# Performance work log

Hardware: AMD Instinct MI355X
Metric: run time of the kernel (lower is better)

## Reference

```python
import jax, jax.numpy as jnp
import numpy as np

DEPTH, HEADS, DH, BUCKET, NHASH = 4, 8, 64, 64, 4
DIM, VOCAB, BATCH, SEQ = 512, 50000, 2, 2048
LN_EPS = 1e-5
SELF_ATTN_VAL = -5e4  # TOKEN_SELF_ATTN_VALUE in reformer_pytorch


def layer_norm(x, s, b):
    mu = x.mean(-1, keepdims=True)
    var = ((x - mu) ** 2).mean(-1, keepdims=True)
    return (x - mu) / jnp.sqrt(var + LN_EPS) * s + b


def sincos(t, dh):
    # FixedPositionalEmbedding: emb = cat(sin, cos) of t x dh/2 angles
    inv = 1.0 / (10000.0 ** (jnp.arange(0, dh, 2, dtype=jnp.float32) / dh))
    ang = jnp.arange(t, dtype=jnp.float32)[:, None] * inv[None, :]
    return jnp.sin(ang), jnp.cos(ang)


def apply_rotary(qk, sin, cos):
    # qk: [B*H, T, DH]; sin/cos: [T, DH/2]; interleaved-pair rotary as in reformer_pytorch
    sin2 = jnp.repeat(sin, 2, axis=-1)[None]
    cos2 = jnp.repeat(cos, 2, axis=-1)[None]
    xr = qk.reshape(qk.shape[0], qk.shape[1], -1, 2)
    rot = jnp.stack((-xr[..., 1], xr[..., 0]), axis=-1).reshape(qk.shape)
    return qk * cos2 + rot * sin2


def lsh_attention(qk, v, rot):
    # qk, v: [B, T, dh] (B = batch*heads, shared-QK); rot: [dh, NHASH, n_buckets//2]
    B, T, dh = qk.shape
    nb = T // BUCKET
    rv = jnp.einsum('btf,fhi->bhti', qk, rot)           # [B, NHASH, T, nb/2]
    rv = jnp.concatenate([rv, -rv], axis=-1)
    buckets = jnp.argmax(rv, axis=-1)                    # [B, NHASH, T]
    buckets = (buckets + (jnp.arange(NHASH) * nb)[None, :, None]).reshape(B, NHASH * T)
    ticker = jnp.arange(NHASH * T) % T
    key = T * buckets + ticker[None, :]                  # unique sort keys
    sticker = jnp.argsort(key, axis=-1)                  # [B, NHASH*T]
    undo = jnp.argsort(sticker, axis=-1)
    st = sticker % T
    sqk = jnp.take_along_axis(qk, st[:, :, None], axis=1)
    sv = jnp.take_along_axis(v, st[:, :, None], axis=1)
    C = NHASH * nb                                       # num chunks, each BUCKET long
    bq_t = st.reshape(B, C, BUCKET)
    bq = sqk.reshape(B, C, BUCKET, dh)
    bv = sv.reshape(B, C, BUCKET, dh)
    bk = bq / jnp.maximum(jnp.linalg.norm(bq, axis=-1, keepdims=True), 1e-12)

    def look_one_back(a):
        return jnp.concatenate([a, jnp.roll(a, 1, axis=1)], axis=2)

    bk, bv, bkv_t = look_one_back(bk), look_one_back(bv), look_one_back(bq_t)
    dots = jnp.einsum('bcie,bcje->bcij', bq, bk) * (dh ** -0.5)
    dots = jnp.where(bq_t[:, :, :, None] == bkv_t[:, :, None, :], SELF_ATTN_VAL, dots)
    lse = jax.nn.logsumexp(dots, axis=-1, keepdims=True)
    p = jnp.exp(dots - lse)
    bo = jnp.einsum('bcij,bcje->bcie', p, bv)
    so = bo.reshape(B, NHASH * T, dh)
    slog = lse.reshape(B, NHASH * T)
    o = jnp.take_along_axis(so, undo[:, :, None], axis=1).reshape(B, NHASH, T, dh)
    lg = jnp.take_along_axis(slog, undo, axis=1).reshape(B, NHASH, T, 1)
    w = jnp.exp(lg - jax.nn.logsumexp(lg, axis=1, keepdims=True))
    return jnp.sum(o * w, axis=1)                        # [B, T, dh]


def attn_block(x, s, bln, Wqk, Wv, Wo, bo, rot, sin, cos):
    b, t, _ = x.shape
    xn = layer_norm(x, s, bln)
    qk = (xn @ Wqk).reshape(b, t, HEADS, DH).transpose(0, 2, 1, 3).reshape(b * HEADS, t, DH)
    v = (xn @ Wv).reshape(b, t, HEADS, DH).transpose(0, 2, 1, 3).reshape(b * HEADS, t, DH)
    qk = apply_rotary(qk, sin, cos)
    o = lsh_attention(qk, v, rot)
    o = o.reshape(b, HEADS, t, DH).transpose(0, 2, 1, 3).reshape(b, t, HEADS * DH)
    return o @ Wo + bo


def ff_block(x, s, b, W1, b1, W2, b2):
    xn = layer_norm(x, s, b)
    return jax.nn.gelu(xn @ W1 + b1, approximate=False) @ W2 + b2


def reference(x, token_emb, ln1_s, ln1_b, Wqk, Wv, Wo, bo, ln2_s, ln2_b, W1, b1, W2, b2, rotations, lnf_s, lnf_b, Wf1, bf1, Wout, bout):
    e = token_emb[x]                                     # [B, T, DIM]
    sin, cos = sincos(x.shape[1], DH)
    x1 = x2 = e                                          # reversible twin streams
    for i in range(DEPTH):
        x1 = x1 + attn_block(x2, ln1_s[i], ln1_b[i], Wqk[i], Wv[i], Wo[i], bo[i], rotations[i], sin, cos)
        x2 = x2 + ff_block(x1, ln2_s[i], ln2_b[i], W1[i], b1[i], W2[i], b2[i])
    h = layer_norm((x1 + x2) * 0.5, lnf_s, lnf_b)
    h = h.mean(axis=1)
    h = jax.nn.relu(h @ Wf1 + bf1)
    return h @ Wout + bout


def setup_inputs():
    key = jax.random.key(0)
    ks = jax.random.split(key, 10)
    nb = SEQ // BUCKET
    s = 0.02
    return {
        'x': jax.random.randint(ks[0], (BATCH, SEQ), 0, VOCAB),
        'token_emb': jax.random.normal(ks[1], (VOCAB, DIM), jnp.float32) * s,
        'ln1_s': jnp.ones((DEPTH, DIM), jnp.float32),
        'ln1_b': jnp.zeros((DEPTH, DIM), jnp.float32),
        'Wqk': jax.random.normal(ks[2], (DEPTH, DIM, HEADS * DH), jnp.float32) * s,
        'Wv': jax.random.normal(ks[3], (DEPTH, DIM, HEADS * DH), jnp.float32) * s,
        'Wo': jax.random.normal(ks[4], (DEPTH, HEADS * DH, DIM), jnp.float32) * s,
        'bo': jnp.zeros((DEPTH, DIM), jnp.float32),
        'ln2_s': jnp.ones((DEPTH, DIM), jnp.float32),
        'ln2_b': jnp.zeros((DEPTH, DIM), jnp.float32),
        'W1': jax.random.normal(ks[5], (DEPTH, DIM, 4 * DIM), jnp.float32) * s,
        'b1': jnp.zeros((DEPTH, 4 * DIM), jnp.float32),
        'W2': jax.random.normal(ks[6], (DEPTH, 4 * DIM, DIM), jnp.float32) * s,
        'b2': jnp.zeros((DEPTH, DIM), jnp.float32),
        'rotations': jax.random.normal(ks[7], (DEPTH, DH, NHASH, nb // 2), jnp.float32),
        'lnf_s': jnp.ones((DIM,), jnp.float32),
        'lnf_b': jnp.zeros((DIM,), jnp.float32),
        'Wf1': jax.random.normal(ks[8], (DIM, 256), jnp.float32) * s,
        'bf1': jnp.zeros((256,), jnp.float32),
        'Wout': jax.random.normal(ks[9], (256, 1), jnp.float32) * s,
        'bout': jnp.zeros((1,), jnp.float32),
    }
```

## Files before the change

### kernel.cpp

```cpp
#include <hip/hip_runtime.h>
#include <math.h>

#define TSEQ   2048
#define DIMM   512
#define NHEAD  8
#define DHD    64
#define BHD    16
#define NHASHK 4
#define CHUNKS 128
#define FFD    2048
#define NROWS  4096

#define OFF_WQK 0
#define OFF_WV  262144
#define OFF_WO  524288
#define OFF_W1  786432
#define OFF_W2  1835008
#define WT_TOT  2883584

typedef unsigned short u16;
typedef _Float16 f16;
typedef __attribute__((ext_vector_type(8))) _Float16 f16x8;
typedef __attribute__((ext_vector_type(4))) float f32x4;
typedef __attribute__((ext_vector_type(8))) unsigned short ushort8v;
typedef __attribute__((ext_vector_type(4))) unsigned short ushort4v;

__device__ inline u16 h16(float f) {
  union { f16 h; u16 u; } x;
  x.h = (f16)f;
  return x.u;
}
__device__ inline float f16f(u16 u) {
  union { u16 u; f16 h; } x;
  x.u = u;
  return (float)x.h;
}
__device__ inline f16x8 mk8f(unsigned a, unsigned b, unsigned c, unsigned d) {
  union { unsigned u[4]; f16x8 v; } x;
  x.u[0] = a; x.u[1] = b; x.u[2] = c; x.u[3] = d;
  return x.v;
}
__device__ inline float gelu_exact(float v) {
  return 0.5f * v * (1.0f + erff(v * 0.70710678118654752f));
}
__device__ inline int swz128(int row, int colbyte) {
  return row * 128 + (colbyte ^ ((row & 7) << 4));
}
#define VT(d, k) ((d) * 264 + (((d) & 32) ? 8 : 0) + ((k) << 1))

__global__ __launch_bounds__(128) void k_embed(const int* __restrict__ x, const float* __restrict__ emb,
                                               float* __restrict__ x1, float* __restrict__ x2) {
  int row = blockIdx.x;
  int tok = x[row];
  float4 v = ((const float4*)(emb + (size_t)tok * DIMM))[threadIdx.x];
  ((float4*)(x1 + (size_t)row * DIMM))[threadIdx.x] = v;
  ((float4*)(x2 + (size_t)row * DIMM))[threadIdx.x] = v;
}

__global__ __launch_bounds__(256) void k_sincos(float* __restrict__ sin_t, float* __restrict__ cos_t) {
  int idx = blockIdx.x * 256 + threadIdx.x;
  int t = idx >> 5, i = idx & 31;
  float inv = powf(10000.0f, -(float)(2 * i) / 64.0f);
  float ang = (float)t * inv;
  sin_t[idx] = sinf(ang);
  cos_t[idx] = cosf(ang);
}

__global__ __launch_bounds__(256) void k_layernorm(const float* __restrict__ x, const float* __restrict__ g,
                                                   const float* __restrict__ b, u16* __restrict__ dst) {
  int row = blockIdx.x, tid = threadIdx.x;
  const float* xr = x + (size_t)row * DIMM;
  float v0 = xr[tid], v1 = xr[tid + 256];
  int lane = tid & 63, w = tid >> 6;
  __shared__ float red[8];
  float s = v0 + v1;
#pragma unroll
  for (int o = 32; o; o >>= 1) s += __shfl_xor(s, o);
  if (lane == 0) red[w] = s;
  __syncthreads();
  float mu = (red[0] + red[1] + red[2] + red[3]) * (1.0f / DIMM);
  float d0 = v0 - mu, d1 = v1 - mu;
  float q = d0 * d0 + d1 * d1;
#pragma unroll
  for (int o = 32; o; o >>= 1) q += __shfl_xor(q, o);
  if (lane == 0) red[4 + w] = q;
  __syncthreads();
  float var = (red[4] + red[5] + red[6] + red[7]) * (1.0f / DIMM);
  float rstd = 1.0f / sqrtf(var + 1e-5f);
  size_t base = (size_t)row * DIMM;
  dst[base + tid] = h16(d0 * rstd * g[tid] + b[tid]);
  dst[base + tid + 256] = h16(d1 * rstd * g[tid + 256] + b[tid + 256]);
}

__global__ __launch_bounds__(256) void k_prep(const float* __restrict__ Wqk, const float* __restrict__ Wv,
                                              const float* __restrict__ Wo, const float* __restrict__ W1,
                                              const float* __restrict__ W2, const float* __restrict__ rot,
                                              u16* __restrict__ wt16, u16* __restrict__ rt16) {
  __shared__ float tile[32][33];
  const int L = blockIdx.x / 2820;
  const int idx = blockIdx.x - L * 2820;
  Wqk += (size_t)L * 262144;
  Wv  += (size_t)L * 262144;
  Wo  += (size_t)L * 262144;
  W1  += (size_t)L * 1048576;
  W2  += (size_t)L * 1048576;
  rot += (size_t)L * 4096;
  u16* wt = wt16 + (size_t)L * WT_TOT;
  u16* rt = rt16 + (size_t)L * 4096;
  const float* src;
  u16* dh;
  int K, N, k0, n0;
  if (idx < 768) {
    int w = idx >> 8, r = idx & 255;
    K = 512; N = 512; k0 = (r >> 4) << 5; n0 = (r & 15) << 5;
    src = (w == 0) ? Wqk : (w == 1) ? Wv : Wo;
    dh = wt + (size_t)w * 262144;
  } else if (idx < 1792) {
    int r = idx - 768;
    K = 512; N = 2048; k0 = (r >> 6) << 5; n0 = (r & 63) << 5;
    src = W1; dh = wt + OFF_W1;
  } else if (idx < 2816) {
    int r = idx - 1792;
    K = 2048; N = 512; k0 = (r >> 4) << 5; n0 = (r & 15) << 5;
    src = W2; dh = wt + OFF_W2;
  } else {
    int r = idx - 2816;
    K = 64; N = 64; k0 = (r >> 1) << 5; n0 = (r & 1) << 5;
    src = rot; dh = rt;
  }
  const int t = threadIdx.x;
  const int r = t >> 3, c4 = (t & 7) << 2;
  float4 v = *(const float4*)&src[(size_t)(k0 + r) * N + n0 + c4];
  tile[r][c4] = v.x; tile[r][c4 + 1] = v.y; tile[r][c4 + 2] = v.z; tile[r][c4 + 3] = v.w;
  __syncthreads();
  u16 hs[4];
#pragma unroll
  for (int i = 0; i < 4; ++i) hs[i] = h16(tile[c4 + i][r]);
  size_t o = (size_t)(n0 + r) * K + k0 + c4;
  *(ushort4v*)&dh[o] = (ushort4v){hs[0], hs[1], hs[2], hs[3]};
}

template <int BM, int STORE>
__global__ __launch_bounds__(256) void k_gemm16(
    const u16* __restrict__ A, const u16* __restrict__ Bt,
    const float* __restrict__ bias, float* __restrict__ out,
    u16* __restrict__ out16, u16* __restrict__ qk16, u16* __restrict__ v16,
    int K, int N,
    const float* __restrict__ sin_t, const float* __restrict__ cos_t,
    const u16* __restrict__ rt16, int* __restrict__ bucket) {
  constexpr int MF = BM / 32;
  constexpr int ACH = BM / 32;
  __shared__ __align__(16) char AsB[BM * 128];
  __shared__ __align__(16) char BsB[64 * 128];
  const int bm = blockIdx.x * BM, bn = blockIdx.y << 6;
  const int tid = threadIdx.x, lane = tid & 63, wid = tid >> 6;
  const int wm = (wid >> 1) * (BM / 2), wn = (wid & 1) << 5;
  const int l16 = lane & 15, g = lane >> 4;
  f32x4 acc[MF][2];
#pragma unroll
  for (int m = 0; m < MF; ++m) { acc[m][0] = (f32x4){0,0,0,0}; acc[m][1] = (f32x4){0,0,0,0}; }

  const int srow = tid >> 3;
  const int scolb = (tid & 7) << 4;
  const u16* ap = A + (size_t)(bm + srow) * K + ((tid & 7) << 3);
  const u16* bp = Bt + (size_t)(bn + srow) * K + ((tid & 7) << 3);

  ushort8v paA[ACH], pbA[2], paB[ACH], pbB[2];
#pragma unroll
  for (int i = 0; i < ACH; ++i) paA[i] = *(const ushort8v*)(ap + (size_t)(i << 5) * K);
#pragma unroll
  for (int i = 0; i < 2; ++i) pbA[i] = *(const ushort8v*)(bp + (size_t)(i << 5) * K);
#pragma unroll
  for (int i = 0; i < ACH; ++i) paB[i] = *(const ushort8v*)(ap + (size_t)(i << 5) * K + 64);
#pragma unroll
  for (int i = 0; i < 2; ++i) pbB[i] = *(const ushort8v*)(bp + (size_t)(i << 5) * K + 64);

  auto gstep = [&](ushort8v (&PA)[ACH], ushort8v (&PB)[2], int S) {
#pragma unroll
    for (int i = 0; i < ACH; ++i)
      *(ushort8v*)(AsB + swz128(srow + (i << 5), scolb)) = PA[i];
#pragma unroll
    for (int i = 0; i < 2; ++i)
      *(ushort8v*)(BsB + swz128(srow + (i << 5), scolb)) = PB[i];
    __syncthreads();
    const int kf = (S + 2) << 6;
    if (kf < K) {
#pragma unroll
      for (int i = 0; i < ACH; ++i) PA[i] = *(const ushort8v*)(ap + (size_t)(i << 5) * K + kf);
#pragma unroll
      for (int i = 0; i < 2; ++i) PB[i] = *(const ushort8v*)(bp + (size_t)(i << 5) * K + kf);
    }
    f16x8 af[MF][2], bfr[2][2];
#pragma unroll
    for (int m = 0; m < MF; ++m)
#pragma unroll
      for (int ks = 0; ks < 2; ++ks)
        af[m][ks] = *(const f16x8*)(AsB + swz128(wm + (m << 4) + l16, ((ks << 2) + g) << 4));
#pragma unroll
    for (int n = 0; n < 2; ++n)
#pragma unroll
      for (int ks = 0; ks < 2; ++ks)
        bfr[n][ks] = *(const f16x8*)(BsB + swz128(wn + (n << 4) + l16, ((ks << 2) + g) << 4));
#pragma unroll
    for (int m = 0; m < MF; ++m)
#pragma unroll
      for (int n = 0; n < 2; ++n)
#pragma unroll
        for (int ks = 0; ks < 2; ++ks)
          acc[m][n] = __builtin_amdgcn_mfma_f32_16x16x32_f16(af[m][ks], bfr[n][ks], acc[m][n], 0, 0, 0);
    __syncthreads();
  };

  const int nsteps = K >> 6;
  for (int s = 0; s < nsteps; s += 2) {
    gstep(paA, pbA, s);
    gstep(paB, pbB, s + 1);
  }

  const bool do_bucket = (STORE == 5) && (bn < 512);
  ushort8v prt0{}, prt1{};
  if (do_bucket) {
    int i0 = tid, i1 = tid + 256;
    prt0 = *(const ushort8v*)(rt16 + (i0 >> 3) * 64 + ((i0 & 7) << 3));
    prt1 = *(const ushort8v*)(rt16 + (i1 >> 3) * 64 + ((i1 & 7) << 3));
  }

#pragma unroll
  for (int m = 0; m < MF; ++m) {
#pragma unroll
    for (int n = 0; n < 2; ++n) {
      const int gn = bn + wn + (n << 4) + l16;
      float bv = 0.f;
      if (STORE == 1 || STORE == 4) bv = bias[gn];
#pragma unroll
      for (int r = 0; r < 4; ++r) {
        const int gm = bm + wm + (m << 4) + (g << 2) + r;
        float val = acc[m][n][r];
        if (STORE == 1) {
          out[(size_t)gm * N + gn] += val + bv;
        } else if (STORE == 4) {
          out16[(size_t)gm * N + gn] = h16(gelu_exact(val + bv));
        } else {
          const float pv = __shfl_xor(val, 1);
          const int bb = gm >> 11, tt = gm & (TSEQ - 1);
          if (gn < 512) {
            const int hh = gn >> 6, dd = gn & 63;
            const int ip = dd >> 1;
            float cz = cos_t[tt * 32 + ip], sz = sin_t[tt * 32 + ip];
            float o = (dd & 1) ? (val * cz + pv * sz) : (val * cz - pv * sz);
            u16 oh = h16(o);
            qk16[((size_t)((bb * NHEAD + hh) * TSEQ + tt)) * DHD + dd] = oh;
            *(u16*)(AsB + swz128(gm - bm, dd << 1)) = oh;
          } else {
            const int gnn = gn - 512;
            const int hh = gnn >> 6, dd = gnn & 63;
            v16[((size_t)((bb * NHEAD + hh) * TSEQ + tt)) * DHD + dd] = h16(val);
          }
        }
      }
    }
  }

  if (do_bucket) {
    {
      int i0 = tid, i1 = tid + 256;
      *(ushort8v*)(BsB + swz128(i0 >> 3, (i0 & 7) << 4)) = prt0;
      *(ushort8v*)(BsB + swz128(i1 >> 3, (i1 & 7) << 4)) = prt1;
    }
    __syncthreads();
    const int bwm = (wid >> 1) << 5;
    const int bwn = (wid & 1) << 5;
    f32x4 bacc[2][2];
#pragma unroll
    for (int m = 0; m < 2; ++m) { bacc[m][0] = (f32x4){0,0,0,0}; bacc[m][1] = (f32x4){0,0,0,0}; }
#pragma unroll
    for (int ks = 0; ks < 2; ++ks) {
      f16x8 bfr[2];
#pragma unroll
      for (int n = 0; n < 2; ++n)
        bfr[n] = *(const f16x8*)(BsB + swz128(bwn + (n << 4) + l16, (ks << 6) + (g << 4)));
#pragma unroll
      for (int m = 0; m < 2; ++m) {
        f16x8 afr = *(const f16x8*)(AsB + swz128(bwm + (m << 4) + l16, (ks << 6) + (g << 4)));
#pragma unroll
        for (int n = 0; n < 2; ++n)
          bacc[m][n] = __builtin_amdgcn_mfma_f32_16x16x32_f16(afr, bfr[n], bacc[m][n], 0, 0, 0);
      }
    }
    const int bb = bm >> 11;
    const int hh = bn >> 6;
#pragma unroll
    for (int m = 0; m < 2; ++m)
#pragma unroll
      for (int n = 0; n < 2; ++n) {
        const int hcol = (bwn >> 4) + n;
#pragma unroll
        for (int r = 0; r < 4; ++r) {
          float v = bacc[m][n][r];
          float best = v; int bi = l16;
          if (-v > best) { best = -v; bi = 16 + l16; }
#pragma unroll
          for (int o = 1; o < 16; o <<= 1) {
            float ob = __shfl_xor(best, o);
            int obi = __shfl_xor(bi, o);
            if (ob > best || (ob == best && obi < bi)) { best = ob; bi = obi; }
          }
          if (l16 == 0) {
            int t = (bm & (TSEQ - 1)) + bwm + (m << 4) + (g << 2) + r;
            bucket[((size_t)((bb * NHEAD + hh) * NHASHK) + hcol) * TSEQ + t] = bi;
          }
        }
      }
  }
}

__global__ __launch_bounds__(256) void k_gemm128(
    const u16* __restrict__ A, const u16* __restrict__ Bt,
    const float* __restrict__ bias, u16* __restrict__ out16,
    int K, int N) {
  __shared__ __align__(16) char AsB[128 * 128];
  __shared__ __align__(16) char BsB[128 * 128];
  const int bm = blockIdx.x << 7, bn = blockIdx.y << 7;
  const int tid = threadIdx.x, lane = tid & 63, wid = tid >> 6;
  const int wm = (wid >> 1) << 6, wn = (wid & 1) << 6;
  const int l16 = lane & 15, g = lane >> 4;
  f32x4 acc[4][4];
#pragma unroll
  for (int m = 0; m < 4; ++m)
#pragma unroll
    for (int n = 0; n < 4; ++n) acc[m][n] = (f32x4){0.f, 0.f, 0.f, 0.f};

  const int srow = tid >> 3;
  const int scolb = (tid & 7) << 4;
  const u16* ap = A + (size_t)(bm + srow) * K + ((tid & 7) << 3);
  const u16* bp = Bt + (size_t)(bn + srow) * K + ((tid & 7) << 3);

  ushort8v pa[4], pb[4];
#pragma unroll
  for (int i = 0; i < 4; ++i) {
    pa[i] = *(const ushort8v*)(ap + (size_t)(i << 5) * K);
    pb[i] = *(const ushort8v*)(bp + (size_t)(i << 5) * K);
  }

  for (int k0 = 0;;) {
#pragma unroll
    for (int i = 0; i < 4; ++i) {
      *(ushort8v*)(AsB + swz128(srow + (i << 5), scolb)) = pa[i];
      *(ushort8v*)(BsB + swz128(srow + (i << 5), scolb)) = pb[i];
    }
    __syncthreads();
    const int kn = k0 + 64;
    if (kn < K) {
#pragma unroll
      for (int i = 0; i < 4; ++i) {
        pa[i] = *(const ushort8v*)(ap + (size_t)(i << 5) * K + kn);
        pb[i] = *(const ushort8v*)(bp + (size_t)(i << 5) * K + kn);
      }
    }
#pragma unroll
    for (int ks = 0; ks < 2; ++ks) {
      f16x8 af[4], bfr[4];
#pragma unroll
      for (int m = 0; m < 4; ++m)
        af[m] = *(const f16x8*)(AsB + swz128(wm + (m << 4) + l16, ((ks << 2) + g) << 4));
#pragma unroll
      for (int n = 0; n < 4; ++n)
        bfr[n] = *(const f16x8*)(BsB + swz128(wn + (n << 4) + l16, ((ks << 2) + g) << 4));
#pragma unroll
      for (int m = 0; m < 4; ++m)
#pragma unroll
        for (int n = 0; n < 4; ++n)
          acc[m][n] = __builtin_amdgcn_mfma_f32_16x16x32_f16(af[m], bfr[n], acc[m][n], 0, 0, 0);
    }
    if (kn >= K) break;
    __syncthreads();
    k0 = kn;
  }

#pragma unroll
  for (int m = 0; m < 4; ++m) {
#pragma unroll
    for (int n = 0; n < 4; ++n) {
      const int gn = bn + wn + (n << 4) + l16;
      const float bv = bias[gn];
#pragma unroll
      for (int r = 0; r < 4; ++r) {
        const int gm = bm + wm + (m << 4) + (g << 2) + r;
        out16[(size_t)gm * N + gn] = h16(gelu_exact(acc[m][n][r] + bv));
      }
    }
  }
}

__global__ __launch_bounds__(256) void k_sort(const int* __restrict__ bucket, int* __restrict__ st) {
  __shared__ int hist[256][33];
  __shared__ int chunk[8][32];
  __shared__ int bbase[32];
  const int seg = blockIdx.x;
  const int tid = threadIdx.x;
  const int* bk = bucket + (size_t)seg * TSEQ;
  int4 u0 = *(const int4*)(bk + tid * 8);
  int4 u1 = *(const int4*)(bk + tid * 8 + 4);
  int myb[8] = {u0.x, u0.y, u0.z, u0.w, u1.x, u1.y, u1.z, u1.w};
#pragma unroll
  for (int j = 0; j < 33; ++j) hist[tid][j] = 0;
  __syncthreads();
#pragma unroll
  for (int i = 0; i < 8; ++i) hist[tid][myb[i]]++;
  __syncthreads();
  const int b = tid & 31, c = tid >> 5;
  int ssum = 0;
  for (int g2 = c * 32; g2 < c * 32 + 32; ++g2) ssum += hist[g2][b];
  chunk[c][b] = ssum;
  __syncthreads();
  if (tid < 32) {
    int run = 0;
    for (int cc = 0; cc < 8; ++cc) { int v = chunk[cc][tid]; chunk[cc][tid] = run; run += v; }
    bbase[tid] = run;
  }
  __syncthreads();
  if (tid == 0) {
    int s = 0;
    for (int j = 0; j < 32; ++j) { int v = bbase[j]; bbase[j] = s; s += v; }
  }
  __syncthreads();
  int run = chunk[c][b];
  for (int g2 = c * 32; g2 < c * 32 + 32; ++g2) { int v = hist[g2][b]; hist[g2][b] = run; run += v; }
  __syncthreads();
  int* dst = st + (size_t)seg * TSEQ;
#pragma unroll
  for (int i = 0; i < 8; ++i) {
    int bb2 = myb[i];
    int p = bbase[bb2] + hist[tid][bb2];
    hist[tid][bb2]++;
    dst[p] = tid * 8 + i;
  }
}

__global__ __launch_bounds__(256) void k_attn(const u16* __restrict__ qk16,
                                              const u16* __restrict__ v16,
                                              const int* __restrict__ st,
                                              u16* __restrict__ o4h, float* __restrict__ lg) {
  __shared__ __align__(16) char Kb[128 * 128];
  __shared__ __align__(16) char Vb[64 * 264 + 16];
  __shared__ float inv_norm[128];
  __shared__ int tids[128];
  __shared__ float pn[256];
  const int blk = blockIdx.x;
  const int c = blk & (CHUNKS - 1), bh = blk >> 7;
  const int h = c >> 5;
  const int tid = threadIdx.x, lane = tid & 63, wid = tid >> 6;
  const int l16 = lane & 15, g = lane >> 4;

  if (tid < 128) {
    int cc = (tid < 64) ? c : ((c + CHUNKS - 1) & (CHUNKS - 1));
    tids[tid] = st[bh * (NHASHK * TSEQ) + cc * 64 + (tid & 63)];
  }
  __syncthreads();
  {
    const int r = tid >> 1, hf = tid & 1;
    const u16* qsrc = qk16 + ((size_t)bh * TSEQ + tids[r]) * 64 + hf * 32;
    const u16* vsrc = v16 + ((size_t)bh * TSEQ + tids[r]) * 64 + hf * 32;
    float ss = 0.f;
#pragma unroll
    for (int i = 0; i < 4; ++i) {
      ushort8v u = *(const ushort8v*)(qsrc + i * 8);
      *(ushort8v*)(Kb + swz128(r, hf * 64 + i * 16)) = u;
#pragma unroll
      for (int j = 0; j < 8; ++j) { float f = f16f(u[j]); ss += f * f; }
      ushort8v vv8 = *(const ushort8v*)(vsrc + i * 8);
#pragma unroll
      for (int j = 0; j < 8; ++j)
        *(u16*)(Vb + VT(hf * 32 + i * 8 + j, r)) = vv8[j];
    }
    pn[tid] = ss;
  }
  __syncthreads();
  if (tid < 128) {
    float s2 = pn[2 * tid] + pn[2 * tid + 1];
    inv_norm[tid] = 1.0f / fmaxf(sqrtf(s2), 1e-12f);
  }
  __syncthreads();

  const int qrow = (wid << 4) + l16;
  const int tq = tids[qrow];
  const size_t obase = (size_t)(bh * NHASHK + h) * TSEQ + tq;

  f32x4 accs[8];
#pragma unroll
  for (int i = 0; i < 8; ++i) accs[i] = (f32x4){0, 0, 0, 0};
#pragma unroll
  for (int s = 0; s < 2; ++s) {
    f16x8 qf = *(const f16x8*)(Kb + swz128(qrow, ((s << 2) + g) << 4));
#pragma unroll
    for (int mf = 0; mf < 8; ++mf) {
      f16x8 afr = *(const f16x8*)(Kb + swz128(mf * 16 + l16, ((s << 2) + g) << 4));
      accs[mf] = __builtin_amdgcn_mfma_f32_16x16x32_f16(afr, qf, accs[mf], 0, 0, 0);
    }
  }
  float pv[8][4];
  float mx = -3e38f;
#pragma unroll
  for (int mf = 0; mf < 8; ++mf) {
    float4 invn = *(const float4*)&inv_norm[mf * 16 + g * 4];
    int4 tk = *(const int4*)&tids[mf * 16 + g * 4];
    float inva[4] = {invn.x, invn.y, invn.z, invn.w};
    int tka[4] = {tk.x, tk.y, tk.z, tk.w};
#pragma unroll
    for (int r = 0; r < 4; ++r) {
      float d = accs[mf][r] * inva[r] * 0.125f;
      if (tka[r] == tq) d = -5e4f;
      pv[mf][r] = d;
      mx = fmaxf(mx, d);
    }
  }
  mx = fmaxf(mx, __shfl_xor(mx, 16));
  mx = fmaxf(mx, __shfl_xor(mx, 32));
  float sum = 0.f;
#pragma unroll
  for (int mf = 0; mf < 8; ++mf)
#pragma unroll
    for (int r = 0; r < 4; ++r) {
      float e = __expf(pv[mf][r] - mx);
      pv[mf][r] = e;
      sum += e;
    }
  sum += __shfl_xor(sum, 16);
  sum += __shfl_xor(sum, 32);
  float lse = __logf(sum) + mx;
  float rs = 1.0f / sum;
  if (g == 0) lg[obase] = lse;
  unsigned P2[8][2];
#pragma unroll
  for (int mf = 0; mf < 8; ++mf)
#pragma unroll
    for (int m = 0; m < 2; ++m) {
      float p0 = pv[mf][2 * m] * rs, p1 = pv[mf][2 * m + 1] * rs;
      P2[mf][m] = (unsigned)h16(p0) | ((unsigned)h16(p1) << 16);
    }
  f32x4 acco[4];
#pragma unroll
  for (int i = 0; i < 4; ++i) acco[i] = (f32x4){0, 0, 0, 0};
#pragma unroll
  for (int s = 0; s < 4; ++s) {
    unsigned bw[4];
#pragma unroll
    for (int w = 0; w < 4; ++w) {
      int srl = l16 + (((2 * g + (w >> 1)) & 3) << 4);
      unsigned a0 = __shfl(P2[2 * s][w & 1], srl);
      unsigned a1 = __shfl(P2[2 * s + 1][w & 1], srl);
      bw[w] = (g >> 1) ? a1 : a0;
    }
    f16x8 pb = mk8f(bw[0], bw[1], bw[2], bw[3]);
    const int k0 = s * 32 + g * 8;
#pragma unroll
    for (int mf = 0; mf < 4; ++mf) {
      const int dcol = mf * 16 + l16;
      uint2 v0 = *(const uint2*)(Vb + VT(dcol, k0));
      uint2 v1 = *(const uint2*)(Vb + VT(dcol, k0 + 4));
      f16x8 vf = mk8f(v0.x, v0.y, v1.x, v1.y);
      acco[mf] = __builtin_amdgcn_mfma_f32_16x16x32_f16(vf, pb, acco[mf], 0, 0, 0);
    }
  }
#pragma unroll
  for (int mf = 0; mf < 4; ++mf) {
    ushort4v o4s = {h16(acco[mf][0]), h16(acco[mf][1]), h16(acco[mf][2]), h16(acco[mf][3])};
    *(ushort4v*)&o4h[obase * 64 + mf * 16 + g * 4] = o4s;
  }
}

__global__ __launch_bounds__(256) void k_combine(const u16* __restrict__ o4h, const float* __restrict__ lg,
                                                 u16* __restrict__ ctx16) {
  int tok = blockIdx.x * 4 + (threadIdx.x >> 6);
  int dd = threadIdx.x & 63;
  int bh = tok >> 11, t = tok & (TSEQ - 1);
  size_t base = (size_t)bh * NHASHK * TSEQ + t;
  float l0 = lg[base], l1 = lg[base + TSEQ], l2 = lg[base + 2 * TSEQ], l3 = lg[base + 3 * TSEQ];
  float m = fmaxf(fmaxf(l0, l1), fmaxf(l2, l3));
  float e0 = expf(l0 - m), e1 = expf(l1 - m), e2 = expf(l2 - m), e3 = expf(l3 - m);
  float inv = 1.0f / (e0 + e1 + e2 + e3);
  float o = (e0 * f16f(o4h[base * 64 + dd]) + e1 * f16f(o4h[(base + TSEQ) * 64 + dd]) +
             e2 * f16f(o4h[(base + 2 * TSEQ) * 64 + dd]) + e3 * f16f(o4h[(base + 3 * TSEQ) * 64 + dd])) * inv;
  int b = bh >> 3, hh = bh & 7;
  ctx16[((size_t)(b * TSEQ + t)) * DIMM + hh * DHD + dd] = h16(o);
}

__global__ __launch_bounds__(256) void k_colmean1(const float* __restrict__ x1, const float* __restrict__ x2,
                                                  float* __restrict__ part) {
  const int blk = blockIdx.x;
  const int bb = blk >> 8, ch = blk & 255;
  const int tid = threadIdx.x, lane = tid & 63, w = tid >> 6;
  __shared__ float red[8];
  float a0 = 0.f, a1 = 0.f;
  for (int i = 0; i < 8; ++i) {
    int row = bb * TSEQ + ch * 8 + i;
    size_t base = (size_t)row * DIMM;
    float v0 = 0.5f * (x1[base + tid] + x2[base + tid]);
    float v1 = 0.5f * (x1[base + tid + 256] + x2[base + tid + 256]);
    float s = v0 + v1;
#pragma unroll
    for (int o = 32; o; o >>= 1) s += __shfl_xor(s, o);
    if (lane == 0) red[w] = s;
    __syncthreads();
    float mu = (red[0] + red[1] + red[2] + red[3]) * (1.0f / DIMM);
    float d0 = v0 - mu, d1 = v1 - mu;
    float q = d0 * d0 + d1 * d1;
#pragma unroll
    for (int o = 32; o; o >>= 1) q += __shfl_xor(q, o);
    if (lane == 0) red[4 + w] = q;
    __syncthreads();
    float var = (red[4] + red[5] + red[6] + red[7]) * (1.0f / DIMM);
    float rstd = 1.0f / sqrtf(var + 1e-5f);
    a0 += d0 * rstd;
    a1 += d1 * rstd;
    __syncthreads();
  }
  part[(size_t)blk * DIMM + tid] = a0;
  part[(size_t)blk * DIMM + tid + 256] = a1;
}

__global__ __launch_bounds__(256) void k_colmean2(const float* __restrict__ part,
                                                  const float* __restrict__ g, const float* __restrict__ b,
                                                  float* __restrict__ hm) {
  int gidx = blockIdx.x * 256 + threadIdx.x;
  int oid = gidx >> 3, sub = gidx & 7;
  int bb = oid >> 9, d = oid & 511;
  float s = 0.f;
  for (int c = sub; c < 256; c += 8) s += part[((size_t)(bb * 256 + c)) * DIMM + d];
  s += __shfl_xor(s, 1);
  s += __shfl_xor(s, 2);
  s += __shfl_xor(s, 4);
  if (sub == 0) hm[oid] = s * (1.0f / TSEQ) * g[d] + b[d];
}

__global__ __launch_bounds__(256) void k_head1(const float* __restrict__ hm, const float* __restrict__ Wf1,
                                               float* __restrict__ r1p) {
  int b = blockIdx.x & 1, kc = blockIdx.x >> 1;
  int j = threadIdx.x;
  float acc = 0;
  for (int k = kc * 64; k < kc * 64 + 64; ++k) acc += hm[b * DIMM + k] * Wf1[k * 256 + j];
  r1p[(size_t)(kc * 2 + b) * 256 + j] = acc;
}

__global__ __launch_bounds__(256) void k_head2(const float* __restrict__ r1p, const float* __restrict__ bf1,
                                               const float* __restrict__ Wout, const float* __restrict__ bout,
                                               float* __restrict__ outp) {
  int b = blockIdx.x;
  int tid = threadIdx.x, lane = tid & 63, w = tid >> 6;
  float s = 0.f;
#pragma unroll
  for (int kc = 0; kc < 8; ++kc) s += r1p[(size_t)(kc * 2 + b) * 256 + tid];
  float v = fmaxf(s + bf1[tid], 0.0f) * Wout[tid];
#pragma unroll
  for (int o = 32; o; o >>= 1) v += __shfl_xor(v, o);
  __shared__ float red[4];
  if (lane == 0) red[w] = v;
  __syncthreads();
  if (tid == 0) outp[b] = red[0] + red[1] + red[2] + red[3] + bout[0];
}

extern "C" void kernel_launch(void* const* d_in, const int* in_sizes, int n_in,
                              void* d_out, int out_size, void* d_ws, size_t ws_size,
                              hipStream_t stream) {
  const int*   x         = (const int*)d_in[0];
  const float* token_emb = (const float*)d_in[1];
  const float* ln1_s     = (const float*)d_in[2];
  const float* ln1_b     = (const float*)d_in[3];
  const float* Wqk       = (const float*)d_in[4];
  const float* Wv        = (const float*)d_in[5];
  const float* Wo        = (const float*)d_in[6];
  const float* bo        = (const float*)d_in[7];
  const float* ln2_s     = (const float*)d_in[8];
  const float* ln2_b     = (const float*)d_in[9];
  const float* W1        = (const float*)d_in[10];
  const float* b1        = (const float*)d_in[11];
  const float* W2        = (const float*)d_in[12];
  const float* b2        = (const float*)d_in[13];
  const float* rotations = (const float*)d_in[14];
  const float* lnf_s     = (const float*)d_in[15];
  const float* lnf_b     = (const float*)d_in[16];
  const float* Wf1       = (const float*)d_in[17];
  const float* bf1       = (const float*)d_in[18];
  const float* Wout      = (const float*)d_in[19];
  const float* bout      = (const float*)d_in[20];
  float* out = (float*)d_out;

  char* ws = (char*)d_ws;
  size_t off = 0;
  auto alloc = [&](size_t nbytes) {
    char* p = ws + off;
    off += (nbytes + 255) & ~(size_t)255;
    return p;
  };
  float*  x1     = (float*)alloc((size_t)NROWS * DIMM * 4);
  float*  x2     = (float*)alloc((size_t)NROWS * DIMM * 4);
  u16*    xn16   = (u16*)alloc((size_t)NROWS * DIMM * 2);
  u16*    qk16   = (u16*)alloc((size_t)BHD * TSEQ * DHD * 2);
  u16*    v16    = (u16*)alloc((size_t)BHD * TSEQ * DHD * 2);
  u16*    ffh16  = (u16*)alloc((size_t)NROWS * FFD * 2);
  u16*    o4h    = (u16*)alloc((size_t)BHD * NHASHK * TSEQ * DHD * 2);
  float*  lg     = (float*)alloc((size_t)BHD * NHASHK * TSEQ * 4);
  float*  sin_t  = (float*)alloc((size_t)TSEQ * 32 * 4);
  float*  cos_t  = (float*)alloc((size_t)TSEQ * 32 * 4);
  float*  part   = (float*)alloc((size_t)512 * DIMM * 4);
  float*  hm     = (float*)alloc(2 * DIMM * 4);
  float*  r1p    = (float*)alloc(16 * 256 * 4);
  int*    bucket = (int*)alloc((size_t)BHD * NHASHK * TSEQ * 4);
  int*    st     = (int*)alloc((size_t)BHD * NHASHK * TSEQ * 4);
  u16*    wt16   = (u16*)alloc((size_t)4 * WT_TOT * 2);
  u16*    rott16 = (u16*)alloc((size_t)4 * 64 * 64 * 2);
  u16*    ctx16  = xn16;

  k_embed<<<NROWS, 128, 0, stream>>>(x, token_emb, x1, x2);
  k_sincos<<<(TSEQ * 32) / 256, 256, 0, stream>>>(sin_t, cos_t);
  k_prep<<<4 * 2820, 256, 0, stream>>>(Wqk, Wv, Wo, W1, W2, rotations, wt16, rott16);

  for (int L = 0; L < 4; ++L) {
    u16* wt = wt16 + (size_t)L * WT_TOT;
    u16* rt = rott16 + (size_t)L * 4096;

    k_layernorm<<<NROWS, 256, 0, stream>>>(x2, ln1_s + L * DIMM, ln1_b + L * DIMM, xn16);
    k_gemm16<64, 5><<<dim3(64, 16), 256, 0, stream>>>(
        xn16, wt + OFF_WQK, nullptr, nullptr, nullptr, qk16, v16, 512, 1024, sin_t, cos_t, rt, bucket);
    k_sort<<<BHD * NHASHK, 256, 0, stream>>>(bucket, st);
    k_attn<<<BHD * CHUNKS, 256, 0, stream>>>(qk16, v16, st, o4h, lg);
    k_combine<<<(BHD * TSEQ) / 4, 256, 0, stream>>>(o4h, lg, ctx16);
    k_gemm16<64, 1><<<dim3(64, 8), 256, 0, stream>>>(
        ctx16, wt + OFF_WO, bo + L * DIMM, x1, nullptr, nullptr, nullptr, 512, 512, nullptr, nullptr, nullptr, nullptr);
    k_layernorm<<<NROWS, 256, 0, stream>>>(x1, ln2_s + L * DIMM, ln2_b + L * DIMM, xn16);
    k_gemm128<<<dim3(32, 16), 256, 0, stream>>>(
        xn16, wt + OFF_W1, b1 + L * FFD, ffh16, 512, 2048);
    k_gemm16<64, 1><<<dim3(64, 8), 256, 0, stream>>>(
        ffh16, wt + OFF_W2, b2 + L * DIMM, x2, nullptr, nullptr, nullptr, 2048, 512, nullptr, nullptr, nullptr, nullptr);
  }

  k_colmean1<<<512, 256, 0, stream>>>(x1, x2, part);
  k_colmean2<<<32, 256, 0, stream>>>(part, lnf_s, lnf_b, hm);
  k_head1<<<16, 256, 0, stream>>>(hm, Wf1, r1p);
  k_head2<<<2, 256, 0, stream>>>(r1p, bf1, Wout, bout, out);
}
```

Measured before the change: 504.3 us.

## Use direct global-to-LDS async loads with double-buffered shared memory in gemm16

The 64x64 GEMM kernel now stages A and B tiles straight into double-buffered LDS with global_load_lds instead of prefetching into registers and then writing to shared memory. The load for the next K step is issued right after the barrier, so it overlaps the MFMA work on the current buffer, and each iteration now needs one barrier instead of two. The unused BM template parameter and the GELU store path are removed. LDS use per block doubles, which may lower occupancy, and the swizzle is now applied to the global source addresses, so correctness depends on that mapping matching the layout the fragment reads expect.

```diff
diff --git a/kernel.cpp b/kernel.cpp
--- a/kernel.cpp
+++ b/kernel.cpp
@@ -47,6 +47,12 @@
   return row * 128 + (colbyte ^ ((row & 7) << 4));
 }
 #define VT(d, k) ((d) * 264 + (((d) & 32) ? 8 : 0) + ((k) << 1))
+
+typedef const __attribute__((address_space(1))) unsigned GUx;
+typedef __attribute__((address_space(3))) unsigned LUx;
+__device__ inline void gload16(const void* g, void* l) {
+  __builtin_amdgcn_global_load_lds((GUx*)g, (LUx*)l, 16, 0, 0);
+}
 
 __global__ __launch_bounds__(128) void k_embed(const int* __restrict__ x, const float* __restrict__ emb,
                                                float* __restrict__ x1, float* __restrict__ x2) {
@@ -140,82 +146,67 @@
   *(ushort4v*)&dh[o] = (ushort4v){hs[0], hs[1], hs[2], hs[3]};
 }
 
-template <int BM, int STORE>
+template <int STORE>
 __global__ __launch_bounds__(256) void k_gemm16(
     const u16* __restrict__ A, const u16* __restrict__ Bt,
     const float* __restrict__ bias, float* __restrict__ out,
-    u16* __restrict__ out16, u16* __restrict__ qk16, u16* __restrict__ v16,
+    u16* __restrict__ qk16, u16* __restrict__ v16,
     int K, int N,
     const float* __restrict__ sin_t, const float* __restrict__ cos_t,
     const u16* __restrict__ rt16, int* __restrict__ bucket) {
-  constexpr int MF = BM / 32;
-  constexpr int ACH = BM / 32;
-  __shared__ __align__(16) char AsB[BM * 128];
-  __shared__ __align__(16) char BsB[64 * 128];
-  const int bm = blockIdx.x * BM, bn = blockIdx.y << 6;
+  __shared__ __align__(16) char AsB[2][64 * 128];
+  __shared__ __align__(16) char BsB[2][64 * 128];
+  const int bm = blockIdx.x << 6, bn = blockIdx.y << 6;
   const int tid = threadIdx.x, lane = tid & 63, wid = tid >> 6;
-  const int wm = (wid >> 1) * (BM / 2), wn = (wid & 1) << 5;
+  const int wm = (wid >> 1) << 5, wn = (wid & 1) << 5;
   const int l16 = lane & 15, g = lane >> 4;
-  f32x4 acc[MF][2];
-#pragma unroll
-  for (int m = 0; m < MF; ++m) { acc[m][0] = (f32x4){0,0,0,0}; acc[m][1] = (f32x4){0,0,0,0}; }
-
-  const int srow = tid >> 3;
-  const int scolb = (tid & 7) << 4;
-  const u16* ap = A + (size_t)(bm + srow) * K + ((tid & 7) << 3);
-  const u16* bp = Bt + (size_t)(bn + srow) * K + ((tid & 7) << 3);
-
-  ushort8v paA[ACH], pbA[2], paB[ACH], pbB[2];
-#pragma unroll
-  for (int i = 0; i < ACH; ++i) paA[i] = *(const ushort8v*)(ap + (size_t)(i << 5) * K);
-#pragma unroll
-  for (int i = 0; i < 2; ++i) pbA[i] = *(const ushort8v*)(bp + (size_t)(i << 5) * K);
-#pragma unroll
-  for (int i = 0; i < ACH; ++i) paB[i] = *(const ushort8v*)(ap + (size_t)(i << 5) * K + 64);
-#pragma unroll
-  for (int i = 0; i < 2; ++i) pbB[i] = *(const ushort8v*)(bp + (size_t)(i << 5) * K + 64);
-
-  auto gstep = [&](ushort8v (&PA)[ACH], ushort8v (&PB)[2], int S) {
-#pragma unroll
-    for (int i = 0; i < ACH; ++i)
-      *(ushort8v*)(AsB + swz128(srow + (i << 5), scolb)) = PA[i];
-#pragma unroll
-    for (int i = 0; i < 2; ++i)
-      *(ushort8v*)(BsB + swz128(srow + (i << 5), scolb)) = PB[i];
+  f32x4 acc[2][2];
+#pragma unroll
+  for (int m = 0; m < 2; ++m) { acc[m][0] = (f32x4){0,0,0,0}; acc[m][1] = (f32x4){0,0,0,0}; }
+
+  const int lrow = lane >> 3;
+  const int cele = ((((lane & 7) << 4) ^ (lrow << 4)) >> 1);
+  const int r0 = (wid << 4) + lrow;
+  const int r1 = r0 + 8;
+  const u16* a0 = A + (size_t)(bm + r0) * K + cele;
+  const u16* a1 = A + (size_t)(bm + r1) * K + cele;
+  const u16* b0 = Bt + (size_t)(bn + r0) * K + cele;
+  const u16* b1 = Bt + (size_t)(bn + r1) * K + cele;
+  const int pb0 = (wid << 1) << 10, pb1 = ((wid << 1) + 1) << 10;
+
+  auto STAGE = [&](int buf, int kofs) {
+    gload16(a0 + kofs, &AsB[buf][pb0]);
+    gload16(a1 + kofs, &AsB[buf][pb1]);
+    gload16(b0 + kofs, &BsB[buf][pb0]);
+    gload16(b1 + kofs, &BsB[buf][pb1]);
+  };
+
+  STAGE(0, 0);
+  for (int s = 0;;) {
     __syncthreads();
-    const int kf = (S + 2) << 6;
-    if (kf < K) {
-#pragma unroll
-      for (int i = 0; i < ACH; ++i) PA[i] = *(const ushort8v*)(ap + (size_t)(i << 5) * K + kf);
-#pragma unroll
-      for (int i = 0; i < 2; ++i) PB[i] = *(const ushort8v*)(bp + (size_t)(i << 5) * K + kf);
-    }
-    f16x8 af[MF][2], bfr[2][2];
-#pragma unroll
-    for (int m = 0; m < MF; ++m)
-#pragma unroll
-      for (int ks = 0; ks < 2; ++ks)
-        af[m][ks] = *(const f16x8*)(AsB + swz128(wm + (m << 4) + l16, ((ks << 2) + g) << 4));
-#pragma unroll
-    for (int n = 0; n < 2; ++n)
-#pragma unroll
-      for (int ks = 0; ks < 2; ++ks)
-        bfr[n][ks] = *(const f16x8*)(BsB + swz128(wn + (n << 4) + l16, ((ks << 2) + g) << 4));
-#pragma unroll
-    for (int m = 0; m < MF; ++m)
+    const int kn = (s + 1) << 6;
+    if (kn < K) STAGE((s + 1) & 1, kn);
+    const char* Ab = AsB[s & 1];
+    const char* Bb = BsB[s & 1];
+#pragma unroll
+    for (int ks = 0; ks < 2; ++ks) {
+      f16x8 af[2], bfr[2];
+#pragma unroll
+      for (int m = 0; m < 2; ++m)
+        af[m] = *(const f16x8*)(Ab + swz128(wm + (m << 4) + l16, ((ks << 2) + g) << 4));
 #pragma unroll
       for (int n = 0; n < 2; ++n)
-#pragma unroll
-        for (int ks = 0; ks < 2; ++ks)
-          acc[m][n] = __builtin_amdgcn_mfma_f32_16x16x32_f16(af[m][ks], bfr[n][ks], acc[m][n], 0, 0, 0);
-    __syncthreads();
-  };
-
-  const int nsteps = K >> 6;
-  for (int s = 0; s < nsteps; s += 2) {
-    gstep(paA, pbA, s);
-    gstep(paB, pbB, s + 1);
-  }
+        bfr[n] = *(const f16x8*)(Bb + swz128(wn + (n << 4) + l16, ((ks << 2) + g) << 4));
+#pragma unroll
+      for (int m = 0; m < 2; ++m)
+#pragma unroll
+        for (int n = 0; n < 2; ++n)
+          acc[m][n] = __builtin_amdgcn_mfma_f32_16x16x32_f16(af[m], bfr[n], acc[m][n], 0, 0, 0);
+    }
+    if (kn >= K) break;
+    ++s;
+  }
+  __syncthreads();
 
   const bool do_bucket = (STORE == 5) && (bn < 512);
   ushort8v prt0{}, prt1{};
@@ -226,20 +217,18 @@
   }
 
 #pragma unroll
-  for (int m = 0; m < MF; ++m) {
+  for (int m = 0; m < 2; ++m) {
 #pragma unroll
     for (int n = 0; n < 2; ++n) {
       const int gn = bn + wn + (n << 4) + l16;
       float bv = 0.f;
-      if (STORE == 1 || STORE == 4) bv = bias[gn];
+      if (STORE == 1) bv = bias[gn];
 #pragma unroll
       for (int r = 0; r < 4; ++r) {
         const int gm = bm + wm + (m << 4) + (g << 2) + r;
         float val = acc[m][n][r];
         if (STORE == 1) {
           out[(size_t)gm * N + gn] += val + bv;
-        } else if (STORE == 4) {
-          out16[(size_t)gm * N + gn] = h16(gelu_exact(val + bv));
         } else {
           const float pv = __shfl_xor(val, 1);
           const int bb = gm >> 11, tt = gm & (TSEQ - 1);
@@ -250,7 +239,7 @@
             float o = (dd & 1) ? (val * cz + pv * sz) : (val * cz - pv * sz);
             u16 oh = h16(o);
             qk16[((size_t)((bb * NHEAD + hh) * TSEQ + tt)) * DHD + dd] = oh;
-            *(u16*)(AsB + swz128(gm - bm, dd << 1)) = oh;
+            *(u16*)(&AsB[0][0] + swz128(gm - bm, dd << 1)) = oh;
           } else {
             const int gnn = gn - 512;
             const int hh = gnn >> 6, dd = gnn & 63;
@@ -261,56 +250,58 @@
     }
   }
 
-  if (do_bucket) {
-    {
-      int i0 = tid, i1 = tid + 256;
-      *(ushort8v*)(BsB + swz128(i0 >> 3, (i0 & 7) << 4)) = prt0;
-      *(ushort8v*)(BsB + swz128(i1 >> 3, (i1 & 7) << 4)) = prt1;
-    }
-    __syncthreads();
-    const int bwm = (wid >> 1) << 5;
-    const int bwn = (wid & 1) << 5;
-    f32x4 bacc[2][2];
-#pragma unroll
-    for (int m = 0; m < 2; ++m) { bacc[m][0] = (f32x4){0,0,0,0}; bacc[m][1] = (f32x4){0,0,0,0}; }
-#pragma unroll
-    for (int ks = 0; ks < 2; ++ks) {
-      f16x8 bfr[2];
-#pragma unroll
-      for (int n = 0; n < 2; ++n)
-        bfr[n] = *(const f16x8*)(BsB + swz128(bwn + (n << 4) + l16, (ks << 6) + (g << 4)));
-#pragma unroll
-      for (int m = 0; m < 2; ++m) {
-        f16x8 afr = *(const f16x8*)(AsB + swz128(bwm + (m << 4) + l16, (ks << 6) + (g << 4)));
+  if constexpr (STORE == 5) {
+    if (do_bucket) {
+      {
+        int i0 = tid, i1 = tid + 256;
+        *(ushort8v*)(&BsB[0][0] + swz128(i0 >> 3, (i0 & 7) << 4)) = prt0;
+        *(ushort8v*)(&BsB[0][0] + swz128(i1 >> 3, (i1 & 7) << 4)) = prt1;
+      }
+      __syncthreads();
+      const int bwm = (wid >> 1) << 5;
+      const int bwn = (wid & 1) << 5;
+      f32x4 bacc[2][2];
+#pragma unroll
+      for (int m = 0; m < 2; ++m) { bacc[m][0] = (f32x4){0,0,0,0}; bacc[m][1] = (f32x4){0,0,0,0}; }
+#pragma unroll
+      for (int ks = 0; ks < 2; ++ks) {
+        f16x8 bfr[2];
 #pragma unroll
         for (int n = 0; n < 2; ++n)
-          bacc[m][n] = __builtin_amdgcn_mfma_f32_16x16x32_f16(afr, bfr[n], bacc[m][n], 0, 0, 0);
+          bfr[n] = *(const f16x8*)(&BsB[0][0] + swz128(bwn + (n << 4) + l16, (ks << 6) + (g << 4)));
+#pragma unroll
+        for (int m = 0; m < 2; ++m) {
+          f16x8 afr = *(const f16x8*)(&AsB[0][0] + swz128(bwm + (m << 4) + l16, (ks << 6) + (g << 4)));
+#pragma unroll
+          for (int n = 0; n < 2; ++n)
+            bacc[m][n] = __builtin_amdgcn_mfma_f32_16x16x32_f16(afr, bfr[n], bacc[m][n], 0, 0, 0);
+        }
       }
-    }
-    const int bb = bm >> 11;
-    const int hh = bn >> 6;
-#pragma unroll
-    for (int m = 0; m < 2; ++m)
-#pragma unroll
-      for (int n = 0; n < 2; ++n) {
-        const int hcol = (bwn >> 4) + n;
-#pragma unroll
-        for (int r = 0; r < 4; ++r) {
-          float v = bacc[m][n][r];
-          float best = v; int bi = l16;
-          if (-v > best) { best = -v; bi = 16 + l16; }
-#pragma unroll
-          for (int o = 1; o < 16; o <<= 1) {
-            float ob = __shfl_xor(best, o);
-            int obi = __shfl_xor(bi, o);
-            if (ob > best || (ob == best && obi < bi)) { best = ob; bi = obi; }
-          }
-          if (l16 == 0) {
-            int t = (bm & (TSEQ - 1)) + bwm + (m << 4) + (g << 2) + r;
-            bucket[((size_t)((bb * NHEAD + hh) * NHASHK) + hcol) * TSEQ + t] = bi;
+      const int bb = bm >> 11;
+      const int hh = bn >> 6;
+#pragma unroll
+      for (int m = 0; m < 2; ++m)
+#pragma unroll
+        for (int n = 0; n < 2; ++n) {
+          const int hcol = (bwn >> 4) + n;
+#pragma unroll
+          for (int r = 0; r < 4; ++r) {
+            float v = bacc[m][n][r];
+            float best = v; int bi = l16;
+            if (-v > best) { best = -v; bi = 16 + l16; }
+#pragma unroll
+            for (int o = 1; o < 16; o <<= 1) {
+              float ob = __shfl_xor(best, o);
+              int obi = __shfl_xor(bi, o);
+              if (ob > best || (ob == best && obi < bi)) { best = ob; bi = obi; }
+            }
+            if (l16 == 0) {
+              int t = (bm & (TSEQ - 1)) + bwm + (m << 4) + (g << 2) + r;
+              bucket[((size_t)((bb * NHEAD + hh) * NHASHK) + hcol) * TSEQ + t] = bi;
+            }
           }
         }
-      }
+    }
   }
 }
 
@@ -720,18 +711,18 @@
     u16* rt = rott16 + (size_t)L * 4096;
 
     k_layernorm<<<NROWS, 256, 0, stream>>>(x2, ln1_s + L * DIMM, ln1_b + L * DIMM, xn16);
-    k_gemm16<64, 5><<<dim3(64, 16), 256, 0, stream>>>(
-        xn16, wt + OFF_WQK, nullptr, nullptr, nullptr, qk16, v16, 512, 1024, sin_t, cos_t, rt, bucket);
+    k_gemm16<5><<<dim3(64, 16), 256, 0, stream>>>(
+        xn16, wt + OFF_WQK, nullptr, nullptr, qk16, v16, 512, 1024, sin_t, cos_t, rt, bucket);
     k_sort<<<BHD * NHASHK, 256, 0, stream>>>(bucket, st);
     k_attn<<<BHD * CHUNKS, 256, 0, stream>>>(qk16, v16, st, o4h, lg);
     k_combine<<<(BHD * TSEQ) / 4, 256, 0, stream>>>(o4h, lg, ctx16);
-    k_gemm16<64, 1><<<dim3(64, 8), 256, 0, stream>>>(
-        ctx16, wt + OFF_WO, bo + L * DIMM, x1, nullptr, nullptr, nullptr, 512, 512, nullptr, nullptr, nullptr, nullptr);
+    k_gemm16<1><<<dim3(64, 8), 256, 0, stream>>>(
+        ctx16, wt + OFF_WO, bo + L * DIMM, x1, nullptr, nullptr, 512, 512, nullptr, nullptr, nullptr, nullptr);
     k_layernorm<<<NROWS, 256, 0, stream>>>(x1, ln2_s + L * DIMM, ln2_b + L * DIMM, xn16);
     k_gemm128<<<dim3(32, 16), 256, 0, stream>>>(
         xn16, wt + OFF_W1, b1 + L * FFD, ffh16, 512, 2048);
-    k_gemm16<64, 1><<<dim3(64, 8), 256, 0, stream>>>(
-        ffh16, wt + OFF_W2, b2 + L * DIMM, x2, nullptr, nullptr, nullptr, 2048, 512, nullptr, nullptr, nullptr, nullptr);
+    k_gemm16<1><<<dim3(64, 8), 256, 0, stream>>>(
+        ffh16, wt + OFF_W2, b2 + L * DIMM, x2, nullptr, nullptr, 2048, 512, nullptr, nullptr, nullptr, nullptr);
   }
 
   k_colmean1<<<512, 256, 0, stream>>>(x1, x2, part);
```

After: 523.1 us. +3.7%, slower.
